# Kernel optimization log

Measured on AMD Instinct MI355X. Metric: run time of the kernel, lower is better.

Reference implementation:

```python
import jax, jax.numpy as jnp
import numpy as np

D_MODEL = 1024
NUM_HEADS = 16
HEAD_DIM = D_MODEL // NUM_HEADS


def setup_inputs() -> dict:
    key = jax.random.key(0)
    ks = jax.random.split(key, 5)
    s = 0.02
    x = jax.random.normal(ks[0], (4, 2048, D_MODEL), dtype=jnp.float32)
    W_Q = jax.random.normal(ks[1], (D_MODEL, D_MODEL), dtype=jnp.float32) * s
    W_K = jax.random.normal(ks[2], (D_MODEL, D_MODEL), dtype=jnp.float32) * s
    W_V = jax.random.normal(ks[3], (D_MODEL, D_MODEL), dtype=jnp.float32) * s
    W_O = jax.random.normal(ks[4], (D_MODEL, D_MODEL), dtype=jnp.float32) * s
    return {"x": x, "W_Q": W_Q, "W_K": W_K, "W_V": W_V, "W_O": W_O}


def reference(x, W_Q, W_K, W_V, W_O):
    b, s, d = x.shape
    h, hd = NUM_HEADS, HEAD_DIM
    scale = 1.0 / np.sqrt(hd).astype(np.float32)
    # nn.Linear applies x @ W.T; split heads then transpose -> (b, h, s, hd)
    def split(W):
        return (x @ W.T).reshape(b, s, h, hd).transpose(0, 2, 1, 3)
    Q, K, V = split(W_Q), split(W_K), split(W_V)
    scores = jnp.einsum('bhqd,bhkd->bhqk', Q, K) * scale
    causal = jnp.triu(jnp.ones((s, s), dtype=bool), k=1)
    scores = jnp.where(causal, -jnp.inf, scores)
    weights = jax.nn.softmax(scores, axis=-1)
    ctx = jnp.einsum('bhqk,bhkd->bhqd', weights, V)
    ctx = ctx.transpose(0, 2, 1, 3).reshape(b, s, d)
    return ctx @ W_O.T
```

## Files before the change

kernel.cpp:

```cpp
#include <hip/hip_runtime.h>


#define B_  4
#define S_  2048
#define D_  1024
#define H_  16
#define HD_ 64

typedef __attribute__((ext_vector_type(8))) short bf16x8;
typedef __attribute__((ext_vector_type(4))) float f32x4;

#define MFMA16 __builtin_amdgcn_mfma_f32_16x16x32_bf16

__device__ __forceinline__ unsigned short f2b(float f) {
  unsigned u = __builtin_bit_cast(unsigned, f);
  unsigned r = (u + 0x7FFFu + ((u >> 16) & 1u)) >> 16;
  return (unsigned short)r;
}

__device__ __forceinline__ unsigned cvtpk(float lo, float hi) {
  unsigned r;
  asm("v_cvt_pk_bf16_f32 %0, %1, %2" : "=v"(r) : "v"(lo), "v"(hi));
  return r;
}

__device__ __forceinline__ void gll16(const void* g, const void* l) {
  __builtin_amdgcn_global_load_lds(
      (const __attribute__((address_space(1))) unsigned int*)g,
      (__attribute__((address_space(3))) unsigned int*)l, 16, 0, 0);
}

__global__ __launch_bounds__(256) void cvt_all(
    const float4* __restrict__ x,  const float4* __restrict__ wq,
    const float4* __restrict__ wk, const float4* __restrict__ wv,
    const float4* __restrict__ wo,
    ushort4* __restrict__ xb,  ushort4* __restrict__ wqb,
    ushort4* __restrict__ wkb, ushort4* __restrict__ wvb,
    ushort4* __restrict__ wob)
{
  const int y = blockIdx.y;
  const float4* in; ushort4* out;
  if (y < 8)       { in = x  + (size_t)y * 262144; out = xb  + (size_t)y * 262144; }
  else if (y == 8) { in = wq; out = wqb; }
  else if (y == 9) { in = wk; out = wkb; }
  else if (y == 10){ in = wv; out = wvb; }
  else             { in = wo; out = wob; }
  int i = blockIdx.x * 256 + threadIdx.x;
  float4 v = in[i];
  ushort4 o;
  o.x = f2b(v.x); o.y = f2b(v.y); o.z = f2b(v.z); o.w = f2b(v.w);
  out[i] = o;
}

template<int MODE>
__global__ __launch_bounds__(256) void gemm_bt(
    const unsigned short* __restrict__ A,
    const unsigned short* __restrict__ B0,
    const unsigned short* __restrict__ B1,
    unsigned short* __restrict__ O0,
    unsigned short* __restrict__ O1,
    float* __restrict__ OF)
{
  const int tid  = threadIdx.x;
  const int lane = tid & 63;
  const int w    = tid >> 6;
  const int wm   = w >> 1, wn = w & 1;
  const int r16  = lane & 15, g = lane >> 4;
  const int bm = blockIdx.x, bn = blockIdx.y;

  const unsigned short* Bw = (MODE == 0 && blockIdx.z == 1) ? B1 : B0;
  unsigned short* Ob       = (MODE == 0 && blockIdx.z == 1) ? O1 : O0;

  __shared__ unsigned short As[2][4096];
  __shared__ unsigned short Bs[2][4096];

  const int arow = bm * 128, brow = bn * 128;
  const int srow = lane >> 2, scol = (lane & 3) * 8;

  auto STAGE = [&](int bf_, int k0_) {
    #pragma unroll
    for (int t = 0; t < 2; ++t) {
      const int grow = t*64 + w*16 + srow;
      const int lbas = (t*256 + w*64) * 8;
      gll16(A  + (size_t)(arow + grow)*1024 + k0_ + scol, &As[bf_][lbas]);
      gll16(Bw + (size_t)(brow + grow)*1024 + k0_ + scol, &Bs[bf_][lbas]);
    }
  };

  f32x4 acc[4][4] = {};
  int bf = 0;
  STAGE(0, 0);
  for (int kt = 0; kt < 32; ++kt) {
    __syncthreads();
    if (kt + 1 < 32) STAGE(bf ^ 1, (kt + 1) * 32);
    bf16x8 af[4], bfr[4];
    #pragma unroll
    for (int i = 0; i < 4; ++i)
      af[i]  = *(const bf16x8*)(&As[bf][(wm*64 + i*16 + r16)*32 + g*8]);
    #pragma unroll
    for (int i = 0; i < 4; ++i)
      bfr[i] = *(const bf16x8*)(&Bs[bf][(wn*64 + i*16 + r16)*32 + g*8]);
    #pragma unroll
    for (int i = 0; i < 4; ++i)
      #pragma unroll
      for (int j = 0; j < 4; ++j)
        acc[i][j] = (MODE == 2) ? MFMA16(bfr[j], af[i], acc[i][j], 0, 0, 0)
                                : MFMA16(af[i], bfr[j], acc[i][j], 0, 0, 0);
    bf ^= 1;
  }

  #pragma unroll
  for (int i = 0; i < 4; ++i) {
    #pragma unroll
    for (int j = 0; j < 4; ++j) {
      #pragma unroll
      for (int r = 0; r < 4; ++r) {
        float v = acc[i][j][r];
        if (MODE == 1) {
          int m = arow + wm*64 + i*16 + g*4 + r;
          int n = brow + wn*64 + j*16 + r16;
          OF[(size_t)m * 1024 + n] = v;
        } else if (MODE == 0) {
          int m = arow + wm*64 + i*16 + g*4 + r;
          int n = brow + wn*64 + j*16 + r16;
          float scl = (blockIdx.z == 0) ? 0.18033688f : 1.0f;
          int b = m >> 11, s = m & 2047, h = n >> 6, hd = n & 63;
          Ob[((((size_t)b*H_ + h)*S_) + s)*HD_ + hd] = f2b(v * scl);
        } else {
          int n = brow + wn*64 + j*16 + g*4 + r;
          int m = arow + wm*64 + i*16 + r16;
          int b = m >> 11, s = m & 2047, h = n >> 6, hd = n & 63;
          O0[(((size_t)b*H_ + h)*HD_ + hd)*S_ + s] = f2b(v);
        }
      }
    }
  }
}

__global__ __launch_bounds__(256, 4) void attn_fwd(
    const unsigned short* __restrict__ Q,
    const unsigned short* __restrict__ K,
    const unsigned short* __restrict__ Vt,
    unsigned short* __restrict__ C)
{
  const int tid  = threadIdx.x;
  const int lane = tid & 63;
  const int w    = tid >> 6;
  const int r16  = lane & 15, g = lane >> 4;

  const int l_   = blockIdx.x;
  const int bh   = (l_ & 7) * 8 + ((l_ >> 3) & 7);
  const int px   = l_ >> 6;
  const int bb   = bh >> 4, hh = bh & 15;

  const unsigned short* Qh = Q  + (size_t)bh * S_ * HD_;
  const unsigned short* Kh = K  + (size_t)bh * S_ * HD_;
  const unsigned short* Vh = Vt + (size_t)bh * HD_ * S_;

  __shared__ unsigned short KV[2][2][4096];
  __shared__ unsigned short Pl[4][1024];
  char* Plw = (char*)&Pl[w][0];

  const int rsub = lane >> 3;
  const int csw  = ((lane & 7) ^ rsub) * 8;

  bf16x8 onesf;
  #pragma unroll
  for (int j = 0; j < 8; ++j) onesf[j] = (short)0x3F80;

  auto STAGE = [&](int bf_, int kb_) {
    #pragma unroll
    for (int j = 0; j < 2; ++j) {
      const int tr = w*16 + j*8;
      gll16(Kh + (size_t)(kb_ + tr + rsub)*HD_ + csw, &KV[bf_][0][tr*64]);
      gll16(Vh + (size_t)(tr + rsub)*S_ + kb_ + csw,  &KV[bf_][1][tr*64]);
    }
  };
  auto FR = [&](const unsigned short* base, int row, int c16) -> bf16x8 {
    return *(const bf16x8*)((const char*)base + row*128 + (((c16 ^ (row & 7)) & 7) << 4));
  };
  auto PR = [&](int row, int kc) -> bf16x8 {
    return *(const bf16x8*)(Plw + row*128 + ((kc*64 + g*16) ^ ((row & 7) << 4)));
  };

  int bf = 0;
  STAGE(0, 0);

  #pragma unroll
  for (int ph = 0; ph < 2; ++ph) {
    const int jt = ph ? (31 - px) : px;
    const int q0 = jt * 64;
    const int qw = q0 + w * 16;
    const int nt = jt + 1;

    bf16x8 qf[2];
    #pragma unroll
    for (int dh = 0; dh < 2; ++dh)
      qf[dh] = *(const bf16x8*)(&Qh[(size_t)(qw + r16) * HD_ + dh*32 + g*8]);

    f32x4 oT[4] = {};
    f32x4 oL = {};

    for (int kt = 0; kt < nt; ++kt) {
      const int kb = kt * 64;
      __syncthreads();
      if (kt + 1 < nt)  STAGE(bf ^ 1, kb + 64);
      else if (ph == 0) STAGE(bf ^ 1, 0);
      const unsigned short* Kt = &KV[bf][0][0];
      const unsigned short* Vs = &KV[bf][1][0];

      f32x4 sc[4];
      __builtin_amdgcn_s_setprio(1);
      #pragma unroll
      for (int c = 0; c < 4; ++c) {
        bf16x8 kf0 = FR(Kt, c*16 + r16, g);
        bf16x8 kf1 = FR(Kt, c*16 + r16, 4 + g);
        f32x4 s = {};
        s = MFMA16(kf0, qf[0], s, 0, 0, 0);
        s = MFMA16(kf1, qf[1], s, 0, 0, 0);
        sc[c] = s;
      }
      __builtin_amdgcn_s_setprio(0);

      f32x4 p4[4];
      if (kb + 63 > qw) {
        const int qrow = qw + r16;
        #pragma unroll
        for (int c = 0; c < 4; ++c)
          #pragma unroll
          for (int r = 0; r < 4; ++r)
            p4[c][r] = (kb + c*16 + g*4 + r > qrow) ? 0.f : exp2f(sc[c][r]);
      } else {
        #pragma unroll
        for (int c = 0; c < 4; ++c)
          #pragma unroll
          for (int r = 0; r < 4; ++r)
            p4[c][r] = exp2f(sc[c][r]);
      }
      {
        char* prp = Plw + r16*128;
        const int swz = (r16 & 7) << 4;
        #pragma unroll
        for (int c = 0; c < 4; ++c) {
          uint2 pw;
          pw.x = cvtpk(p4[c][0], p4[c][1]);
          pw.y = cvtpk(p4[c][2], p4[c][3]);
          *(uint2*)(prp + ((c*32 + g*8) ^ swz)) = pw;
        }
      }

      __builtin_amdgcn_s_setprio(1);
      #pragma unroll
      for (int kc = 0; kc < 2; ++kc) {
        bf16x8 pf = PR(r16, kc);
        oL = MFMA16(onesf, pf, oL, 0, 0, 0);
        #pragma unroll
        for (int dn = 0; dn < 4; ++dn) {
          bf16x8 vf = FR(Vs, dn*16 + r16, kc*4 + g);
          oT[dn] = MFMA16(vf, pf, oT[dn], 0, 0, 0);
        }
      }
      __builtin_amdgcn_s_setprio(0);
      bf ^= 1;
    }

    float inv = 1.0f / oL[0];
    int tok = bb * S_ + qw + r16;
    #pragma unroll
    for (int dn = 0; dn < 4; ++dn) {
      uint2 cw;
      cw.x = cvtpk(oT[dn][0] * inv, oT[dn][1] * inv);
      cw.y = cvtpk(oT[dn][2] * inv, oT[dn][3] * inv);
      *(uint2*)(&C[(size_t)tok * D_ + hh*HD_ + dn*16 + g*4]) = cw;
    }
  }
}

extern "C" void kernel_launch(void* const* d_in, const int* in_sizes, int n_in,
                              void* d_out, int out_size, void* d_ws, size_t ws_size,
                              hipStream_t stream) {
  const float* x  = (const float*)d_in[0];
  const float* Wq = (const float*)d_in[1];
  const float* Wk = (const float*)d_in[2];
  const float* Wv = (const float*)d_in[3];
  const float* Wo = (const float*)d_in[4];

  char* ws = (char*)d_ws;
  unsigned short* xb  = (unsigned short*)(ws);
  unsigned short* Wqb = (unsigned short*)(ws + 16777216);
  unsigned short* Wkb = (unsigned short*)(ws + 18874368);
  unsigned short* Wvb = (unsigned short*)(ws + 20971520);
  unsigned short* Wob = (unsigned short*)(ws + 23068672);
  unsigned short* Qb  = (unsigned short*)(ws + 25165824);
  unsigned short* Kb  = (unsigned short*)(ws + 41943040);
  unsigned short* Vtb = (unsigned short*)(ws + 58720256);
  unsigned short* Cb  = (unsigned short*)(ws + 75497472);

  cvt_all<<<dim3(1024, 12), 256, 0, stream>>>(
      (const float4*)x, (const float4*)Wq, (const float4*)Wk,
      (const float4*)Wv, (const float4*)Wo,
      (ushort4*)xb, (ushort4*)Wqb, (ushort4*)Wkb, (ushort4*)Wvb, (ushort4*)Wob);

  gemm_bt<0><<<dim3(64, 8, 2), 256, 0, stream>>>(xb, Wqb, Wkb, Qb, Kb, nullptr);
  gemm_bt<2><<<dim3(64, 8, 1), 256, 0, stream>>>(xb, Wvb, nullptr, Vtb, nullptr, nullptr);
  attn_fwd<<<1024, 256, 0, stream>>>(Qb, Kb, Vtb, Cb);
  gemm_bt<1><<<dim3(64, 8, 1), 256, 0, stream>>>(Cb, Wob, nullptr, nullptr, nullptr, (float*)d_out);
}
```

Before: 190.6 us.

## Unroll double-buffered loops by two with static buffer indices; swizzle GEMM tile order

Both the GEMM and attention main loops are unrolled by two so the LDS double-buffer index is a compile-time constant, which removes dynamic buffer address arithmetic. The attention loop now rounds the tile count up to even and skips the extra tile with a causal guard; that odd trailing iteration still issues an extra K/V load, which may read past the valid causal range. The GEMM also remaps block indices into groups of eight M-tiles to improve L2 reuse of the shared operand. Code size and register pressure increase from the duplicated bodies.

```diff
diff --git a/kernel.cpp b/kernel.cpp
--- a/kernel.cpp
+++ b/kernel.cpp
@@ -52,6 +52,24 @@
   out[i] = o;
 }
 
+#define GSTG(BF, K0) { \
+    _Pragma("unroll") for (int t = 0; t < 2; ++t) { \
+      const int grow_ = t*64 + w*16 + srow; \
+      const int lbas_ = (t*256 + w*64) * 8; \
+      gll16(A  + (size_t)(arow + grow_)*1024 + (K0) + scol, &As[BF][lbas_]); \
+      gll16(Bw + (size_t)(brow + grow_)*1024 + (K0) + scol, &Bs[BF][lbas_]); } }
+
+#define GSTEP(BF, SW) { \
+    bf16x8 af[4], bfr[4]; \
+    _Pragma("unroll") for (int i = 0; i < 4; ++i) \
+      af[i]  = *(const bf16x8*)(&As[BF][(wm*64 + i*16 + r16)*32 + g*8]); \
+    _Pragma("unroll") for (int i = 0; i < 4; ++i) \
+      bfr[i] = *(const bf16x8*)(&Bs[BF][(wn*64 + i*16 + r16)*32 + g*8]); \
+    _Pragma("unroll") for (int i = 0; i < 4; ++i) \
+      _Pragma("unroll") for (int j = 0; j < 4; ++j) \
+        acc[i][j] = (SW) ? MFMA16(bfr[j], af[i], acc[i][j], 0, 0, 0) \
+                         : MFMA16(af[i], bfr[j], acc[i][j], 0, 0, 0); }
+
 template<int MODE>
 __global__ __launch_bounds__(256) void gemm_bt(
     const unsigned short* __restrict__ A,
@@ -66,7 +84,11 @@
   const int w    = tid >> 6;
   const int wm   = w >> 1, wn = w & 1;
   const int r16  = lane & 15, g = lane >> 4;
-  const int bm = blockIdx.x, bn = blockIdx.y;
+
+  const int orig = blockIdx.x + 64 * blockIdx.y;
+  const int t_   = orig >> 3;
+  const int bm   = (orig & 7) * 8 + (t_ & 7);
+  const int bn   = t_ >> 3;
 
   const unsigned short* Bw = (MODE == 0 && blockIdx.z == 1) ? B1 : B0;
   unsigned short* Ob       = (MODE == 0 && blockIdx.z == 1) ? O1 : O0;
@@ -76,37 +98,17 @@
 
   const int arow = bm * 128, brow = bn * 128;
   const int srow = lane >> 2, scol = (lane & 3) * 8;
-
-  auto STAGE = [&](int bf_, int k0_) {
-    #pragma unroll
-    for (int t = 0; t < 2; ++t) {
-      const int grow = t*64 + w*16 + srow;
-      const int lbas = (t*256 + w*64) * 8;
-      gll16(A  + (size_t)(arow + grow)*1024 + k0_ + scol, &As[bf_][lbas]);
-      gll16(Bw + (size_t)(brow + grow)*1024 + k0_ + scol, &Bs[bf_][lbas]);
-    }
-  };
+  constexpr bool SW = (MODE == 2);
 
   f32x4 acc[4][4] = {};
-  int bf = 0;
-  STAGE(0, 0);
-  for (int kt = 0; kt < 32; ++kt) {
+  GSTG(0, 0);
+  for (int kt = 0; kt < 32; kt += 2) {
     __syncthreads();
-    if (kt + 1 < 32) STAGE(bf ^ 1, (kt + 1) * 32);
-    bf16x8 af[4], bfr[4];
-    #pragma unroll
-    for (int i = 0; i < 4; ++i)
-      af[i]  = *(const bf16x8*)(&As[bf][(wm*64 + i*16 + r16)*32 + g*8]);
-    #pragma unroll
-    for (int i = 0; i < 4; ++i)
-      bfr[i] = *(const bf16x8*)(&Bs[bf][(wn*64 + i*16 + r16)*32 + g*8]);
-    #pragma unroll
-    for (int i = 0; i < 4; ++i)
-      #pragma unroll
-      for (int j = 0; j < 4; ++j)
-        acc[i][j] = (MODE == 2) ? MFMA16(bfr[j], af[i], acc[i][j], 0, 0, 0)
-                                : MFMA16(af[i], bfr[j], acc[i][j], 0, 0, 0);
-    bf ^= 1;
+    GSTG(1, (kt + 1) * 32);
+    GSTEP(0, SW);
+    __syncthreads();
+    if (kt + 2 < 32) GSTG(0, (kt + 2) * 32);
+    GSTEP(1, SW);
   }
 
   #pragma unroll
@@ -137,6 +139,52 @@
   }
 }
 
+#define ASTG(BF, KB) { \
+    gll16(Kh + (size_t)((KB) + tr0 +     rsub)*HD_ + csw, &KVb[BF][0][ tr0     *64]); \
+    gll16(Kh + (size_t)((KB) + tr0 + 8 + rsub)*HD_ + csw, &KVb[BF][0][(tr0 + 8)*64]); \
+    gll16(Vh + (size_t)(tr0 +     rsub)*S_ + (KB) + csw,  &KVb[BF][1][ tr0     *64]); \
+    gll16(Vh + (size_t)(tr0 + 8 + rsub)*S_ + (KB) + csw,  &KVb[BF][1][(tr0 + 8)*64]); }
+
+#define ACOMP(BF, KB) { \
+    const int kb_ = (KB); \
+    if (kb_ <= qw) { \
+      f32x4 sc[4]; \
+      __builtin_amdgcn_s_setprio(1); \
+      _Pragma("unroll") for (int c = 0; c < 4; ++c) { \
+        bf16x8 kf0 = *(const bf16x8*)((const char*)&KVb[BF][0][0] + (c*16 + r16)*128 + ((( g      ^ (r16 & 7)) & 7) << 4)); \
+        bf16x8 kf1 = *(const bf16x8*)((const char*)&KVb[BF][0][0] + (c*16 + r16)*128 + ((((4 + g) ^ (r16 & 7)) & 7) << 4)); \
+        f32x4 s_ = {}; \
+        s_ = MFMA16(kf0, qf[0], s_, 0, 0, 0); \
+        s_ = MFMA16(kf1, qf[1], s_, 0, 0, 0); \
+        sc[c] = s_; } \
+      __builtin_amdgcn_s_setprio(0); \
+      f32x4 p4[4]; \
+      if (kb_ + 63 > qw) { \
+        const int qrow_ = qw + r16; \
+        _Pragma("unroll") for (int c = 0; c < 4; ++c) \
+          _Pragma("unroll") for (int r = 0; r < 4; ++r) \
+            p4[c][r] = (kb_ + c*16 + g*4 + r > qrow_) ? 0.f : exp2f(sc[c][r]); \
+      } else { \
+        _Pragma("unroll") for (int c = 0; c < 4; ++c) \
+          _Pragma("unroll") for (int r = 0; r < 4; ++r) \
+            p4[c][r] = exp2f(sc[c][r]); } \
+      { char* prp_ = Plw + r16*128; \
+        const int swz_ = (r16 & 7) << 4; \
+        _Pragma("unroll") for (int c = 0; c < 4; ++c) { \
+          uint2 pw_; \
+          pw_.x = cvtpk(p4[c][0], p4[c][1]); \
+          pw_.y = cvtpk(p4[c][2], p4[c][3]); \
+          *(uint2*)(prp_ + ((c*32 + g*8) ^ swz_)) = pw_; } } \
+      __builtin_amdgcn_s_setprio(1); \
+      _Pragma("unroll") for (int kc = 0; kc < 2; ++kc) { \
+        bf16x8 pf_ = *(const bf16x8*)(Plw + r16*128 + ((kc*64 + g*16) ^ ((r16 & 7) << 4))); \
+        oL = MFMA16(onesf, pf_, oL, 0, 0, 0); \
+        _Pragma("unroll") for (int dn = 0; dn < 4; ++dn) { \
+          bf16x8 vf_ = *(const bf16x8*)((const char*)&KVb[BF][1][0] + (dn*16 + r16)*128 + ((((kc*4 + g) ^ (r16 & 7)) & 7) << 4)); \
+          oT[dn] = MFMA16(vf_, pf_, oT[dn], 0, 0, 0); } } \
+      __builtin_amdgcn_s_setprio(0); \
+    } }
+
 __global__ __launch_bounds__(256, 4) void attn_fwd(
     const unsigned short* __restrict__ Q,
     const unsigned short* __restrict__ K,
@@ -157,41 +205,26 @@
   const unsigned short* Kh = K  + (size_t)bh * S_ * HD_;
   const unsigned short* Vh = Vt + (size_t)bh * HD_ * S_;
 
-  __shared__ unsigned short KV[2][2][4096];
+  __shared__ unsigned short KVb[2][2][4096];
   __shared__ unsigned short Pl[4][1024];
   char* Plw = (char*)&Pl[w][0];
 
   const int rsub = lane >> 3;
   const int csw  = ((lane & 7) ^ rsub) * 8;
+  const int tr0  = w * 16;
 
   bf16x8 onesf;
   #pragma unroll
   for (int j = 0; j < 8; ++j) onesf[j] = (short)0x3F80;
 
-  auto STAGE = [&](int bf_, int kb_) {
-    #pragma unroll
-    for (int j = 0; j < 2; ++j) {
-      const int tr = w*16 + j*8;
-      gll16(Kh + (size_t)(kb_ + tr + rsub)*HD_ + csw, &KV[bf_][0][tr*64]);
-      gll16(Vh + (size_t)(tr + rsub)*S_ + kb_ + csw,  &KV[bf_][1][tr*64]);
-    }
-  };
-  auto FR = [&](const unsigned short* base, int row, int c16) -> bf16x8 {
-    return *(const bf16x8*)((const char*)base + row*128 + (((c16 ^ (row & 7)) & 7) << 4));
-  };
-  auto PR = [&](int row, int kc) -> bf16x8 {
-    return *(const bf16x8*)(Plw + row*128 + ((kc*64 + g*16) ^ ((row & 7) << 4)));
-  };
-
-  int bf = 0;
-  STAGE(0, 0);
+  ASTG(0, 0);
 
   #pragma unroll
   for (int ph = 0; ph < 2; ++ph) {
     const int jt = ph ? (31 - px) : px;
     const int q0 = jt * 64;
     const int qw = q0 + w * 16;
-    const int nt = jt + 1;
+    const int nt = (jt + 2) & ~1;
 
     bf16x8 qf[2];
     #pragma unroll
@@ -201,67 +234,14 @@
     f32x4 oT[4] = {};
     f32x4 oL = {};
 
-    for (int kt = 0; kt < nt; ++kt) {
-      const int kb = kt * 64;
+    for (int kt = 0; kt < nt; kt += 2) {
       __syncthreads();
-      if (kt + 1 < nt)  STAGE(bf ^ 1, kb + 64);
-      else if (ph == 0) STAGE(bf ^ 1, 0);
-      const unsigned short* Kt = &KV[bf][0][0];
-      const unsigned short* Vs = &KV[bf][1][0];
-
-      f32x4 sc[4];
-      __builtin_amdgcn_s_setprio(1);
-      #pragma unroll
-      for (int c = 0; c < 4; ++c) {
-        bf16x8 kf0 = FR(Kt, c*16 + r16, g);
-        bf16x8 kf1 = FR(Kt, c*16 + r16, 4 + g);
-        f32x4 s = {};
-        s = MFMA16(kf0, qf[0], s, 0, 0, 0);
-        s = MFMA16(kf1, qf[1], s, 0, 0, 0);
-        sc[c] = s;
-      }
-      __builtin_amdgcn_s_setprio(0);
-
-      f32x4 p4[4];
-      if (kb + 63 > qw) {
-        const int qrow = qw + r16;
-        #pragma unroll
-        for (int c = 0; c < 4; ++c)
-          #pragma unroll
-          for (int r = 0; r < 4; ++r)
-            p4[c][r] = (kb + c*16 + g*4 + r > qrow) ? 0.f : exp2f(sc[c][r]);
-      } else {
-        #pragma unroll
-        for (int c = 0; c < 4; ++c)
-          #pragma unroll
-          for (int r = 0; r < 4; ++r)
-            p4[c][r] = exp2f(sc[c][r]);
-      }
-      {
-        char* prp = Plw + r16*128;
-        const int swz = (r16 & 7) << 4;
-        #pragma unroll
-        for (int c = 0; c < 4; ++c) {
-          uint2 pw;
-          pw.x = cvtpk(p4[c][0], p4[c][1]);
-          pw.y = cvtpk(p4[c][2], p4[c][3]);
-          *(uint2*)(prp + ((c*32 + g*8) ^ swz)) = pw;
-        }
-      }
-
-      __builtin_amdgcn_s_setprio(1);
-      #pragma unroll
-      for (int kc = 0; kc < 2; ++kc) {
-        bf16x8 pf = PR(r16, kc);
-        oL = MFMA16(onesf, pf, oL, 0, 0, 0);
-        #pragma unroll
-        for (int dn = 0; dn < 4; ++dn) {
-          bf16x8 vf = FR(Vs, dn*16 + r16, kc*4 + g);
-          oT[dn] = MFMA16(vf, pf, oT[dn], 0, 0, 0);
-        }
-      }
-      __builtin_amdgcn_s_setprio(0);
-      bf ^= 1;
+      ASTG(1, (kt + 1) * 64);
+      ACOMP(0, kt * 64);
+      __syncthreads();
+      if (kt + 2 < nt)      { ASTG(0, (kt + 2) * 64); }
+      else if (ph == 0)     { ASTG(0, 0); }
+      ACOMP(1, (kt + 1) * 64);
     }
 
     float inv = 1.0f / oL[0];
```

Measured after the change: 186.6 us. 2.1% less time.
